# Performance work log

Measured on AMD Instinct MI355X. Metric: run time of the kernel, lower is better.

The kernel has to match this reference:

```python
import jax, jax.numpy as jnp
import numpy as np

B, H, SQ, SKV, D = 2, 16, 2048, 2048, 64
SCALE = 8  # sqrt(head_dim)


def setup_inputs() -> dict:
    key = jax.random.key(0)
    kq, kk, kv, km = jax.random.split(key, 4)
    q = jax.random.normal(kq, (B, H, SQ, D), dtype=jnp.float32)
    k = jax.random.normal(kk, (B, H, SKV, D), dtype=jnp.float32)
    v = jax.random.normal(kv, (B, H, SKV, D), dtype=jnp.float32)
    mask = jax.random.normal(km, (1, 1, SQ, SKV), dtype=jnp.float32)
    return {"q": q, "k": k, "v": v, "mask": mask, "scale": SCALE}


def reference(q, k, v, mask, scale):
    # scores: [B, H, SQ, SKV]
    scores = jnp.einsum("bhqd,bhkd->bhqk", q, k) / scale
    scores = scores + mask  # broadcast additive mask
    probs = jax.nn.softmax(scores, axis=-1)
    # hidden: [B, H, SQ, D]
    return jnp.einsum("bhqk,bhkd->bhqd", probs, v)
```

## Files before the change

### kernel.cpp

```cpp
#include <hip/hip_runtime.h>
#include <hip/hip_bf16.h>

#define NB 2
#define NH 16
#define NSQ 2048
#define NSKV 2048
#define ND 64
#define NT (NSKV / 64)
#define LOG2E 1.4426950408889634f
#define BHSTRIDE (NSKV * ND)

typedef __attribute__((ext_vector_type(8))) short bf16x8;
typedef __attribute__((ext_vector_type(4))) float f32x4;
typedef __attribute__((address_space(1))) const unsigned gas_u32;
typedef __attribute__((address_space(3))) unsigned las_u32;

__device__ __forceinline__ short f2bf(float x) {
  union { float f; unsigned u; } c; c.f = x;
  unsigned r = c.u + 0x7fffu + ((c.u >> 16) & 1u);
  return (short)(r >> 16);
}
__device__ __forceinline__ unsigned pack_bf2(float lo, float hi) {
  union { __hip_bfloat162 h; unsigned u; } c;
  c.h = __float22bfloat162_rn(float2{lo, hi});
  return c.u;
}
__device__ __forceinline__ float u2f(unsigned u) {
  union { unsigned u; float f; } c; c.u = u; return c.f;
}
__device__ __forceinline__ float exp2_fast(float x) {
#if __has_builtin(__builtin_amdgcn_exp2f)
  return __builtin_amdgcn_exp2f(x);
#else
  return exp2f(x);
#endif
}

__device__ __forceinline__ int kvmap(int x) {
  return (x & 3) | (((x >> 4) & 1) << 2) | (((x >> 2) & 1) << 3)
       | (((x >> 3) & 1) << 4) | (x & 32);
}

__global__ void prep_k(const float* __restrict__ K, short* __restrict__ Kp) {
  const int bh = blockIdx.y, tile = blockIdx.x, tid = (int)threadIdx.x;
#pragma unroll
  for (int h = 0; h < 2; ++h) {
    const int u    = tid + h * 256;
    const int nt   = u >> 7, kc = (u >> 6) & 1, lane = u & 63;
    const int prow = nt * 16 + (lane & 15);
    const float* src = K + ((size_t)bh * NSKV + tile * 64 + kvmap(prow)) * ND
                         + kc * 32 + (lane >> 4) * 8;
    float4 a = *(const float4*)src, b = *(const float4*)(src + 4);
    bf16x8 w;
    w[0]=f2bf(a.x); w[1]=f2bf(a.y); w[2]=f2bf(a.z); w[3]=f2bf(a.w);
    w[4]=f2bf(b.x); w[5]=f2bf(b.y); w[6]=f2bf(b.z); w[7]=f2bf(b.w);
    *(bf16x8*)(Kp + (size_t)bh * BHSTRIDE + (size_t)tile * 4096 + u * 8) = w;
  }
}

__global__ void prep_vt(const float* __restrict__ V, short* __restrict__ Vp) {
  __shared__ float T[64][65];
  const int kv0 = blockIdx.x * 64;
  const int bh  = blockIdx.y;
  const int t   = (int)threadIdx.x;
  const float* src = V + ((size_t)bh * NSKV + kv0) * ND;
#pragma unroll
  for (int i = 0; i < 4; ++i) {
    float4 v = *(const float4*)(src + (size_t)((t >> 4) + 16 * i) * ND + (t & 15) * 4);
    T[(t >> 4) + 16 * i][(t & 15) * 4 + 0] = v.x;
    T[(t >> 4) + 16 * i][(t & 15) * 4 + 1] = v.y;
    T[(t >> 4) + 16 * i][(t & 15) * 4 + 2] = v.z;
    T[(t >> 4) + 16 * i][(t & 15) * 4 + 3] = v.w;
  }
  __syncthreads();
  const int d = t >> 2, c = t & 3;
  bf16x8 w0, w1;
#pragma unroll
  for (int j = 0; j < 8; ++j) w0[j] = f2bf(T[c * 16 + j][d]);
#pragma unroll
  for (int j = 0; j < 8; ++j) w1[j] = f2bf(T[c * 16 + 8 + j][d]);
  const int frag  = (d >> 4) * 2 + (c >> 1);
  const int lane0 = (((2 * c) & 3) << 4) | (d & 15);
  const int lane1 = (((2 * c + 1) & 3) << 4) | (d & 15);
  short* dstb = Vp + (size_t)bh * BHSTRIDE + (size_t)blockIdx.x * 4096 + frag * 512;
  *(bf16x8*)(dstb + lane0 * 8) = w0;
  *(bf16x8*)(dstb + lane1 * 8) = w1;
}

__global__ void prep_mt(const float* __restrict__ M, unsigned short* __restrict__ Mt) {
  const int qt = blockIdx.x, kt = blockIdx.y, t = (int)threadIdx.x;
  const int rl = t >> 4, c = t & 15;
  const int row = qt * 16 + rl;
  float4 v = *(const float4*)(M + (size_t)row * NSKV + kt * 64 + c * 4);
  const int nt   = 2 * (c >> 3) + (c & 1);
  const int lq   = (c >> 1) & 3;
  const int lane = lq * 16 + rl;
  ushort4 o;
  o.x = (unsigned short)f2bf(LOG2E * v.x);
  o.y = (unsigned short)f2bf(LOG2E * v.y);
  o.z = (unsigned short)f2bf(LOG2E * v.z);
  o.w = (unsigned short)f2bf(LOG2E * v.w);
  *(ushort4*)(Mt + (((size_t)qt * 32 + kt) * 64 + lane) * 16 + nt * 4) = o;
}

__global__ __launch_bounds__(256, 2)
void attn_fwd(const float* __restrict__ Q, const short* __restrict__ Kp,
              const short* __restrict__ Vp, const unsigned short* __restrict__ Mt,
              const void* __restrict__ scale_p, float* __restrict__ O)
{
  const int lin = (int)blockIdx.x + ((int)blockIdx.y << 4);
  const int swz = ((lin & 7) << 6) | (lin >> 3);
  const int qb  = swz & 15;
  const int bh  = swz >> 4;

  const int tid = (int)threadIdx.x;
  const int wv  = tid >> 6;
  const int ln  = tid & 63;
  const int l16 = ln & 15;
  const int lq  = ln >> 4;

  float scale_v;
  {
    union { int i; float f; } u;
    u.i = ((const int*)scale_p)[0];
    float af = fabsf(u.f);
    scale_v = (af >= 1e-6f && af <= 1e6f) ? u.f : (float)u.i;
  }
  const float qmul = LOG2E / scale_v;

  const int q0 = qb * 128;
  const short* Kb = Kp + (size_t)bh * BHSTRIDE;
  const short* Vb = Vp + (size_t)bh * BHSTRIDE;

  __shared__ short Kl[2][4096];
  __shared__ short Vl[2][4096];

  bf16x8 qf[2][2];
#pragma unroll
  for (int qs = 0; qs < 2; ++qs) {
    const float* qrow = Q + ((size_t)bh * NSQ + q0 + wv * 32 + qs * 16 + l16) * ND;
#pragma unroll
    for (int kc = 0; kc < 2; ++kc) {
      const float4* p = (const float4*)(qrow + kc * 32 + lq * 8);
      float4 a = p[0], b = p[1];
      bf16x8 f;
      f[0]=f2bf(a.x*qmul); f[1]=f2bf(a.y*qmul); f[2]=f2bf(a.z*qmul); f[3]=f2bf(a.w*qmul);
      f[4]=f2bf(b.x*qmul); f[5]=f2bf(b.y*qmul); f[6]=f2bf(b.z*qmul); f[7]=f2bf(b.w*qmul);
      qf[qs][kc] = f;
    }
  }

  f32x4 oa[2][4];
  f32x4 lacc[2];
#pragma unroll
  for (int qs = 0; qs < 2; ++qs) {
#pragma unroll
    for (int dt = 0; dt < 4; ++dt) { f32x4 z = {0.f,0.f,0.f,0.f}; oa[qs][dt] = z; }
    f32x4 z = {0.f,0.f,0.f,0.f}; lacc[qs] = z;
  }

  bf16x8 ones;
#pragma unroll
  for (int j = 0; j < 8; ++j) ones[j] = (short)0x3F80;

  const unsigned short* M0 = Mt + (size_t)(qb * 8 + wv * 2) * 32768 + (size_t)ln * 16;
  const unsigned short* M1 = M0 + 32768;

  auto mload = [&](int t, float4* mf0, float4* mf1) {
    const unsigned short* p0 = M0 + (size_t)t * 1024;
    const unsigned short* p1 = M1 + (size_t)t * 1024;
    uint4 a0 = *(const uint4*)p0, b0 = *(const uint4*)(p0 + 8);
    uint4 a1 = *(const uint4*)p1, b1 = *(const uint4*)(p1 + 8);
    const unsigned u0[8] = {a0.x,a0.y,a0.z,a0.w,b0.x,b0.y,b0.z,b0.w};
    const unsigned u1[8] = {a1.x,a1.y,a1.z,a1.w,b1.x,b1.y,b1.z,b1.w};
#pragma unroll
    for (int nt = 0; nt < 4; ++nt) {
      mf0[nt] = float4{u2f(u0[nt*2] << 16), u2f(u0[nt*2] & 0xffff0000u),
                       u2f(u0[nt*2+1] << 16), u2f(u0[nt*2+1] & 0xffff0000u)};
      mf1[nt] = float4{u2f(u1[nt*2] << 16), u2f(u1[nt*2] & 0xffff0000u),
                       u2f(u1[nt*2+1] << 16), u2f(u1[nt*2+1] & 0xffff0000u)};
    }
  };

  auto stage = [&](int t, int buf) {
    const short* ks = Kb + (size_t)t * 4096;
    const short* vs = Vb + (size_t)t * 4096;
#pragma unroll
    for (int i = 0; i < 2; ++i) {
      const int chunk = wv * 2 + i;
      __builtin_amdgcn_global_load_lds((gas_u32*)(ks + chunk * 512 + ln * 8),
                                       (las_u32*)&Kl[buf][chunk * 512], 16, 0, 0);
      __builtin_amdgcn_global_load_lds((gas_u32*)(vs + chunk * 512 + ln * 8),
                                       (las_u32*)&Vl[buf][chunk * 512], 16, 0, 0);
    }
  };

  auto subtile = [&](bf16x8 (&kf)[4][2], bf16x8 (&vf)[4][2], int qs, float4* mf) {
    f32x4 s[4];
    __builtin_amdgcn_s_setprio(1);
#pragma unroll
    for (int nt = 0; nt < 4; ++nt) {
      f32x4 a = *(const f32x4*)&mf[nt];
      a = __builtin_amdgcn_mfma_f32_16x16x32_bf16(kf[nt][0], qf[qs][0], a, 0, 0, 0);
      a = __builtin_amdgcn_mfma_f32_16x16x32_bf16(kf[nt][1], qf[qs][1], a, 0, 0, 0);
      s[nt] = a;
    }
    __builtin_amdgcn_s_setprio(0);
#pragma unroll
    for (int nt = 0; nt < 4; ++nt) {
      s[nt][0] = exp2_fast(s[nt][0]);
      s[nt][1] = exp2_fast(s[nt][1]);
      s[nt][2] = exp2_fast(s[nt][2]);
      s[nt][3] = exp2_fast(s[nt][3]);
    }
    bf16x8 pa[2];
#pragma unroll
    for (int kc = 0; kc < 2; ++kc) {
      union { unsigned u[4]; bf16x8 v; } w;
      w.u[0] = pack_bf2(s[2*kc][0],   s[2*kc][1]);
      w.u[1] = pack_bf2(s[2*kc][2],   s[2*kc][3]);
      w.u[2] = pack_bf2(s[2*kc+1][0], s[2*kc+1][1]);
      w.u[3] = pack_bf2(s[2*kc+1][2], s[2*kc+1][3]);
      pa[kc] = w.v;
    }
    __builtin_amdgcn_s_setprio(1);
#pragma unroll
    for (int kc = 0; kc < 2; ++kc) {
#pragma unroll
      for (int dt = 0; dt < 4; ++dt)
        oa[qs][dt] = __builtin_amdgcn_mfma_f32_16x16x32_bf16(pa[kc], vf[dt][kc], oa[qs][dt], 0, 0, 0);
      lacc[qs] = __builtin_amdgcn_mfma_f32_16x16x32_bf16(pa[kc], ones, lacc[qs], 0, 0, 0);
    }
    __builtin_amdgcn_s_setprio(0);
  };

  auto tile = [&](int t, int buf, float4 (&mc0)[4], float4 (&mc1)[4],
                  float4 (&mn0)[4], float4 (&mn1)[4]) {
    if (t + 1 < NT) {
      stage(t + 1, buf ^ 1);
      mload(t + 1, mn0, mn1);
    }
    bf16x8 kf[4][2], vf[4][2];
#pragma unroll
    for (int nt = 0; nt < 4; ++nt)
#pragma unroll
      for (int kc = 0; kc < 2; ++kc) {
        kf[nt][kc] = *(const bf16x8*)&Kl[buf][(nt * 2 + kc) * 512 + ln * 8];
        vf[nt][kc] = *(const bf16x8*)&Vl[buf][(nt * 2 + kc) * 512 + ln * 8];
      }
    subtile(kf, vf, 0, mc0);
    subtile(kf, vf, 1, mc1);
    __syncthreads();
  };

  float4 mA0[4], mA1[4], mB0[4], mB1[4];
  stage(0, 0);
  mload(0, mA0, mA1);
  __syncthreads();

  for (int t = 0; t < NT; t += 2) {
    tile(t,     0, mA0, mA1, mB0, mB1);
    tile(t + 1, 1, mB0, mB1, mA0, mA1);
  }

#pragma unroll
  for (int qs = 0; qs < 2; ++qs)
#pragma unroll
    for (int r = 0; r < 4; ++r) {
      const float inv = 1.0f / lacc[qs][r];
      float* orow = O + ((size_t)bh * NSQ + q0 + wv * 32 + qs * 16 + lq * 4 + r) * ND;
#pragma unroll
      for (int dt = 0; dt < 4; ++dt)
        orow[dt * 16 + l16] = oa[qs][dt][r] * inv;
    }
}

extern "C" void kernel_launch(void* const* d_in, const int* in_sizes, int n_in,
                              void* d_out, int out_size, void* d_ws, size_t ws_size,
                              hipStream_t stream) {
  const float* q     = (const float*)d_in[0];
  const float* k     = (const float*)d_in[1];
  const float* v     = (const float*)d_in[2];
  const float* mask  = (const float*)d_in[3];
  const void*  scale = (const void*)d_in[4];
  float* out = (float*)d_out;

  const size_t NELEM = (size_t)NB * NH * NSKV * ND;
  short* Kpk = (short*)d_ws;
  short* Vpk = Kpk + NELEM;
  unsigned short* Mtl = (unsigned short*)(Vpk + NELEM);

  prep_k<<<dim3(NSKV / 64, NB * NH), 256, 0, stream>>>(k, Kpk);
  prep_vt<<<dim3(NSKV / 64, NB * NH), 256, 0, stream>>>(v, Vpk);
  prep_mt<<<dim3(NSQ / 16, NSKV / 64), 256, 0, stream>>>(mask, Mtl);

  dim3 grid(NSQ / 128, NB * NH);
  attn_fwd<<<grid, 256, 0, stream>>>(q, Kpk, Vpk, Mtl, scale, out);
}
```

Before: 72.34 us.

## Use 512-thread blocks with one 16-row query slice per wave

```diff
diff --git a/kernel.cpp b/kernel.cpp
--- a/kernel.cpp
+++ b/kernel.cpp
@@ -103,15 +103,15 @@
   *(ushort4*)(Mt + (((size_t)qt * 32 + kt) * 64 + lane) * 16 + nt * 4) = o;
 }
 
-__global__ __launch_bounds__(256, 2)
+__global__ __launch_bounds__(512, 4)
 void attn_fwd(const float* __restrict__ Q, const short* __restrict__ Kp,
               const short* __restrict__ Vp, const unsigned short* __restrict__ Mt,
               const void* __restrict__ scale_p, float* __restrict__ O)
 {
-  const int lin = (int)blockIdx.x + ((int)blockIdx.y << 4);
-  const int swz = ((lin & 7) << 6) | (lin >> 3);
-  const int qb  = swz & 15;
-  const int bh  = swz >> 4;
+  const int lin = (int)blockIdx.x;
+  const int j   = lin & 7, m = lin >> 3;
+  const int qb  = 2 * j + (m & 1);
+  const int bh  = m >> 1;
 
   const int tid = (int)threadIdx.x;
   const int wv  = tid >> 6;
@@ -135,10 +135,9 @@
   __shared__ short Kl[2][4096];
   __shared__ short Vl[2][4096];
 
-  bf16x8 qf[2][2];
-#pragma unroll
-  for (int qs = 0; qs < 2; ++qs) {
-    const float* qrow = Q + ((size_t)bh * NSQ + q0 + wv * 32 + qs * 16 + l16) * ND;
+  bf16x8 qf[2];
+  {
+    const float* qrow = Q + ((size_t)bh * NSQ + q0 + wv * 16 + l16) * ND;
 #pragma unroll
     for (int kc = 0; kc < 2; ++kc) {
       const float4* p = (const float4*)(qrow + kc * 32 + lq * 8);
@@ -146,63 +145,62 @@
       bf16x8 f;
       f[0]=f2bf(a.x*qmul); f[1]=f2bf(a.y*qmul); f[2]=f2bf(a.z*qmul); f[3]=f2bf(a.w*qmul);
       f[4]=f2bf(b.x*qmul); f[5]=f2bf(b.y*qmul); f[6]=f2bf(b.z*qmul); f[7]=f2bf(b.w*qmul);
-      qf[qs][kc] = f;
-    }
-  }
-
-  f32x4 oa[2][4];
-  f32x4 lacc[2];
-#pragma unroll
-  for (int qs = 0; qs < 2; ++qs) {
-#pragma unroll
-    for (int dt = 0; dt < 4; ++dt) { f32x4 z = {0.f,0.f,0.f,0.f}; oa[qs][dt] = z; }
-    f32x4 z = {0.f,0.f,0.f,0.f}; lacc[qs] = z;
-  }
+      qf[kc] = f;
+    }
+  }
+
+  f32x4 oa[4];
+  f32x4 lacc;
+#pragma unroll
+  for (int dt = 0; dt < 4; ++dt) { f32x4 z = {0.f,0.f,0.f,0.f}; oa[dt] = z; }
+  { f32x4 z = {0.f,0.f,0.f,0.f}; lacc = z; }
 
   bf16x8 ones;
 #pragma unroll
-  for (int j = 0; j < 8; ++j) ones[j] = (short)0x3F80;
-
-  const unsigned short* M0 = Mt + (size_t)(qb * 8 + wv * 2) * 32768 + (size_t)ln * 16;
-  const unsigned short* M1 = M0 + 32768;
-
-  auto mload = [&](int t, float4* mf0, float4* mf1) {
+  for (int j2 = 0; j2 < 8; ++j2) ones[j2] = (short)0x3F80;
+
+  const unsigned short* M0 = Mt + (size_t)(qb * 8 + wv) * 32768 + (size_t)ln * 16;
+
+  union MU { uint4 q[2]; unsigned u[8]; };
+
+  auto mload = [&](int t, MU& mu) {
     const unsigned short* p0 = M0 + (size_t)t * 1024;
-    const unsigned short* p1 = M1 + (size_t)t * 1024;
-    uint4 a0 = *(const uint4*)p0, b0 = *(const uint4*)(p0 + 8);
-    uint4 a1 = *(const uint4*)p1, b1 = *(const uint4*)(p1 + 8);
-    const unsigned u0[8] = {a0.x,a0.y,a0.z,a0.w,b0.x,b0.y,b0.z,b0.w};
-    const unsigned u1[8] = {a1.x,a1.y,a1.z,a1.w,b1.x,b1.y,b1.z,b1.w};
-#pragma unroll
-    for (int nt = 0; nt < 4; ++nt) {
-      mf0[nt] = float4{u2f(u0[nt*2] << 16), u2f(u0[nt*2] & 0xffff0000u),
-                       u2f(u0[nt*2+1] << 16), u2f(u0[nt*2+1] & 0xffff0000u)};
-      mf1[nt] = float4{u2f(u1[nt*2] << 16), u2f(u1[nt*2] & 0xffff0000u),
-                       u2f(u1[nt*2+1] << 16), u2f(u1[nt*2+1] & 0xffff0000u)};
-    }
+    mu.q[0] = *(const uint4*)p0;
+    mu.q[1] = *(const uint4*)(p0 + 8);
   };
 
   auto stage = [&](int t, int buf) {
     const short* ks = Kb + (size_t)t * 4096;
     const short* vs = Vb + (size_t)t * 4096;
-#pragma unroll
-    for (int i = 0; i < 2; ++i) {
-      const int chunk = wv * 2 + i;
-      __builtin_amdgcn_global_load_lds((gas_u32*)(ks + chunk * 512 + ln * 8),
-                                       (las_u32*)&Kl[buf][chunk * 512], 16, 0, 0);
-      __builtin_amdgcn_global_load_lds((gas_u32*)(vs + chunk * 512 + ln * 8),
-                                       (las_u32*)&Vl[buf][chunk * 512], 16, 0, 0);
-    }
+    __builtin_amdgcn_global_load_lds((gas_u32*)(ks + wv * 512 + ln * 8),
+                                     (las_u32*)&Kl[buf][wv * 512], 16, 0, 0);
+    __builtin_amdgcn_global_load_lds((gas_u32*)(vs + wv * 512 + ln * 8),
+                                     (las_u32*)&Vl[buf][wv * 512], 16, 0, 0);
   };
 
-  auto subtile = [&](bf16x8 (&kf)[4][2], bf16x8 (&vf)[4][2], int qs, float4* mf) {
+  auto tile = [&](int t, int buf, MU& mc, MU& mn) {
+    if (t + 1 < NT) {
+      stage(t + 1, buf ^ 1);
+      mload(t + 1, mn);
+    }
+    bf16x8 kf[4][2], vf[4][2];
+#pragma unroll
+    for (int nt = 0; nt < 4; ++nt)
+#pragma unroll
+      for (int kc = 0; kc < 2; ++kc) {
+        kf[nt][kc] = *(const bf16x8*)&Kl[buf][(nt * 2 + kc) * 512 + ln * 8];
+        vf[nt][kc] = *(const bf16x8*)&Vl[buf][(nt * 2 + kc) * 512 + ln * 8];
+      }
     f32x4 s[4];
     __builtin_amdgcn_s_setprio(1);
 #pragma unroll
     for (int nt = 0; nt < 4; ++nt) {
-      f32x4 a = *(const f32x4*)&mf[nt];
-      a = __builtin_amdgcn_mfma_f32_16x16x32_bf16(kf[nt][0], qf[qs][0], a, 0, 0, 0);
-      a = __builtin_amdgcn_mfma_f32_16x16x32_bf16(kf[nt][1], qf[qs][1], a, 0, 0, 0);
+      const unsigned w0 = mc.u[nt * 2], w1 = mc.u[nt * 2 + 1];
+      f32x4 a;
+      a[0] = u2f(w0 << 16); a[1] = u2f(w0 & 0xffff0000u);
+      a[2] = u2f(w1 << 16); a[3] = u2f(w1 & 0xffff0000u);
+      a = __builtin_amdgcn_mfma_f32_16x16x32_bf16(kf[nt][0], qf[0], a, 0, 0, 0);
+      a = __builtin_amdgcn_mfma_f32_16x16x32_bf16(kf[nt][1], qf[1], a, 0, 0, 0);
       s[nt] = a;
     }
     __builtin_amdgcn_s_setprio(0);
@@ -228,51 +226,31 @@
     for (int kc = 0; kc < 2; ++kc) {
 #pragma unroll
       for (int dt = 0; dt < 4; ++dt)
-        oa[qs][dt] = __builtin_amdgcn_mfma_f32_16x16x32_bf16(pa[kc], vf[dt][kc], oa[qs][dt], 0, 0, 0);
-      lacc[qs] = __builtin_amdgcn_mfma_f32_16x16x32_bf16(pa[kc], ones, lacc[qs], 0, 0, 0);
+        oa[dt] = __builtin_amdgcn_mfma_f32_16x16x32_bf16(pa[kc], vf[dt][kc], oa[dt], 0, 0, 0);
+      lacc = __builtin_amdgcn_mfma_f32_16x16x32_bf16(pa[kc], ones, lacc, 0, 0, 0);
     }
     __builtin_amdgcn_s_setprio(0);
-  };
-
-  auto tile = [&](int t, int buf, float4 (&mc0)[4], float4 (&mc1)[4],
-                  float4 (&mn0)[4], float4 (&mn1)[4]) {
-    if (t + 1 < NT) {
-      stage(t + 1, buf ^ 1);
-      mload(t + 1, mn0, mn1);
-    }
-    bf16x8 kf[4][2], vf[4][2];
-#pragma unroll
-    for (int nt = 0; nt < 4; ++nt)
-#pragma unroll
-      for (int kc = 0; kc < 2; ++kc) {
-        kf[nt][kc] = *(const bf16x8*)&Kl[buf][(nt * 2 + kc) * 512 + ln * 8];
-        vf[nt][kc] = *(const bf16x8*)&Vl[buf][(nt * 2 + kc) * 512 + ln * 8];
-      }
-    subtile(kf, vf, 0, mc0);
-    subtile(kf, vf, 1, mc1);
     __syncthreads();
   };
 
-  float4 mA0[4], mA1[4], mB0[4], mB1[4];
+  MU mA, mB;
   stage(0, 0);
-  mload(0, mA0, mA1);
+  mload(0, mA);
   __syncthreads();
 
   for (int t = 0; t < NT; t += 2) {
-    tile(t,     0, mA0, mA1, mB0, mB1);
-    tile(t + 1, 1, mB0, mB1, mA0, mA1);
-  }
-
-#pragma unroll
-  for (int qs = 0; qs < 2; ++qs)
-#pragma unroll
-    for (int r = 0; r < 4; ++r) {
-      const float inv = 1.0f / lacc[qs][r];
-      float* orow = O + ((size_t)bh * NSQ + q0 + wv * 32 + qs * 16 + lq * 4 + r) * ND;
-#pragma unroll
-      for (int dt = 0; dt < 4; ++dt)
-        orow[dt * 16 + l16] = oa[qs][dt][r] * inv;
-    }
+    tile(t,     0, mA, mB);
+    tile(t + 1, 1, mB, mA);
+  }
+
+#pragma unroll
+  for (int r = 0; r < 4; ++r) {
+    const float inv = 1.0f / lacc[r];
+    float* orow = O + ((size_t)bh * NSQ + q0 + wv * 16 + lq * 4 + r) * ND;
+#pragma unroll
+    for (int dt = 0; dt < 4; ++dt)
+      orow[dt * 16 + l16] = oa[dt][r] * inv;
+  }
 }
 
 extern "C" void kernel_launch(void* const* d_in, const int* in_sizes, int n_in,
@@ -294,6 +272,5 @@
   prep_vt<<<dim3(NSKV / 64, NB * NH), 256, 0, stream>>>(v, Vpk);
   prep_mt<<<dim3(NSQ / 16, NSKV / 64), 256, 0, stream>>>(mask, Mtl);
 
-  dim3 grid(NSQ / 128, NB * NH);
-  attn_fwd<<<grid, 256, 0, stream>>>(q, Kpk, Vpk, Mtl, scale, out);
-}
+  attn_fwd<<<dim3(512), 512, 0, stream>>>(q, Kpk, Vpk, Mtl, scale, out);
+}
```

New measurement: 77.87 us. 7.6% more time.

## Pack two heads per 512-thread block and defer mask unpacking to use

Applied to the files above, without the earlier changes.

```diff
diff --git a/kernel.cpp b/kernel.cpp
--- a/kernel.cpp
+++ b/kernel.cpp
@@ -103,21 +103,24 @@
   *(ushort4*)(Mt + (((size_t)qt * 32 + kt) * 64 + lane) * 16 + nt * 4) = o;
 }
 
-__global__ __launch_bounds__(256, 2)
+__global__ __launch_bounds__(512, 2)
 void attn_fwd(const float* __restrict__ Q, const short* __restrict__ Kp,
               const short* __restrict__ Vp, const unsigned short* __restrict__ Mt,
               const void* __restrict__ scale_p, float* __restrict__ O)
 {
-  const int lin = (int)blockIdx.x + ((int)blockIdx.y << 4);
-  const int swz = ((lin & 7) << 6) | (lin >> 3);
+  const int lin = (int)blockIdx.x;
+  const int swz = ((lin & 7) << 5) | (lin >> 3);
   const int qb  = swz & 15;
-  const int bh  = swz >> 4;
+  const int bhp = swz >> 4;
 
   const int tid = (int)threadIdx.x;
   const int wv  = tid >> 6;
+  const int wg  = wv >> 2;
+  const int wl  = wv & 3;
   const int ln  = tid & 63;
   const int l16 = ln & 15;
   const int lq  = ln >> 4;
+  const int bh  = bhp * 2 + wg;
 
   float scale_v;
   {
@@ -129,16 +132,18 @@
   const float qmul = LOG2E / scale_v;
 
   const int q0 = qb * 128;
-  const short* Kb = Kp + (size_t)bh * BHSTRIDE;
-  const short* Vb = Vp + (size_t)bh * BHSTRIDE;
-
-  __shared__ short Kl[2][4096];
-  __shared__ short Vl[2][4096];
+  const short* Kb0 = Kp + (size_t)(bhp * 2)     * BHSTRIDE;
+  const short* Kb1 = Kp + (size_t)(bhp * 2 + 1) * BHSTRIDE;
+  const short* Vb0 = Vp + (size_t)(bhp * 2)     * BHSTRIDE;
+  const short* Vb1 = Vp + (size_t)(bhp * 2 + 1) * BHSTRIDE;
+
+  __shared__ short Ksh[2][2][4096];
+  __shared__ short Vsh[2][2][4096];
 
   bf16x8 qf[2][2];
 #pragma unroll
   for (int qs = 0; qs < 2; ++qs) {
-    const float* qrow = Q + ((size_t)bh * NSQ + q0 + wv * 32 + qs * 16 + l16) * ND;
+    const float* qrow = Q + ((size_t)bh * NSQ + q0 + wl * 32 + qs * 16 + l16) * ND;
 #pragma unroll
     for (int kc = 0; kc < 2; ++kc) {
       const float4* p = (const float4*)(qrow + kc * 32 + lq * 8);
@@ -163,44 +168,45 @@
 #pragma unroll
   for (int j = 0; j < 8; ++j) ones[j] = (short)0x3F80;
 
-  const unsigned short* M0 = Mt + (size_t)(qb * 8 + wv * 2) * 32768 + (size_t)ln * 16;
+  const unsigned short* M0 = Mt + (size_t)(qb * 8 + wl * 2) * 32768 + (size_t)ln * 16;
   const unsigned short* M1 = M0 + 32768;
 
-  auto mload = [&](int t, float4* mf0, float4* mf1) {
+  union MU { uint4 q[2]; unsigned u[8]; };
+
+  auto mload = [&](int t, MU& m0, MU& m1) {
     const unsigned short* p0 = M0 + (size_t)t * 1024;
     const unsigned short* p1 = M1 + (size_t)t * 1024;
-    uint4 a0 = *(const uint4*)p0, b0 = *(const uint4*)(p0 + 8);
-    uint4 a1 = *(const uint4*)p1, b1 = *(const uint4*)(p1 + 8);
-    const unsigned u0[8] = {a0.x,a0.y,a0.z,a0.w,b0.x,b0.y,b0.z,b0.w};
-    const unsigned u1[8] = {a1.x,a1.y,a1.z,a1.w,b1.x,b1.y,b1.z,b1.w};
-#pragma unroll
-    for (int nt = 0; nt < 4; ++nt) {
-      mf0[nt] = float4{u2f(u0[nt*2] << 16), u2f(u0[nt*2] & 0xffff0000u),
-                       u2f(u0[nt*2+1] << 16), u2f(u0[nt*2+1] & 0xffff0000u)};
-      mf1[nt] = float4{u2f(u1[nt*2] << 16), u2f(u1[nt*2] & 0xffff0000u),
-                       u2f(u1[nt*2+1] << 16), u2f(u1[nt*2+1] & 0xffff0000u)};
-    }
+    m0.q[0] = *(const uint4*)p0;
+    m0.q[1] = *(const uint4*)(p0 + 8);
+    m1.q[0] = *(const uint4*)p1;
+    m1.q[1] = *(const uint4*)(p1 + 8);
   };
 
   auto stage = [&](int t, int buf) {
-    const short* ks = Kb + (size_t)t * 4096;
-    const short* vs = Vb + (size_t)t * 4096;
-#pragma unroll
-    for (int i = 0; i < 2; ++i) {
-      const int chunk = wv * 2 + i;
-      __builtin_amdgcn_global_load_lds((gas_u32*)(ks + chunk * 512 + ln * 8),
-                                       (las_u32*)&Kl[buf][chunk * 512], 16, 0, 0);
-      __builtin_amdgcn_global_load_lds((gas_u32*)(vs + chunk * 512 + ln * 8),
-                                       (las_u32*)&Vl[buf][chunk * 512], 16, 0, 0);
+#pragma unroll
+    for (int j = 0; j < 4; ++j) {
+      const int c    = wv * 4 + j;
+      const int g2   = c >> 4;
+      const int rem  = c & 15;
+      const int isV  = rem >> 3;
+      const int off8 = (rem & 7) * 512;
+      const short* kb = g2 ? Kb1 : Kb0;
+      const short* vb = g2 ? Vb1 : Vb0;
+      const short* src = (isV ? vb : kb) + (size_t)t * 4096 + off8 + ln * 8;
+      short* dst = isV ? &Vsh[g2][buf][off8] : &Ksh[g2][buf][off8];
+      __builtin_amdgcn_global_load_lds((gas_u32*)src, (las_u32*)dst, 16, 0, 0);
     }
   };
 
-  auto subtile = [&](bf16x8 (&kf)[4][2], bf16x8 (&vf)[4][2], int qs, float4* mf) {
+  auto subtile = [&](bf16x8 (&kf)[4][2], bf16x8 (&vf)[4][2], int qs, MU& mc) {
     f32x4 s[4];
     __builtin_amdgcn_s_setprio(1);
 #pragma unroll
     for (int nt = 0; nt < 4; ++nt) {
-      f32x4 a = *(const f32x4*)&mf[nt];
+      const unsigned w0 = mc.u[nt * 2], w1 = mc.u[nt * 2 + 1];
+      f32x4 a;
+      a[0] = u2f(w0 << 16); a[1] = u2f(w0 & 0xffff0000u);
+      a[2] = u2f(w1 << 16); a[3] = u2f(w1 & 0xffff0000u);
       a = __builtin_amdgcn_mfma_f32_16x16x32_bf16(kf[nt][0], qf[qs][0], a, 0, 0, 0);
       a = __builtin_amdgcn_mfma_f32_16x16x32_bf16(kf[nt][1], qf[qs][1], a, 0, 0, 0);
       s[nt] = a;
@@ -234,8 +240,7 @@
     __builtin_amdgcn_s_setprio(0);
   };
 
-  auto tile = [&](int t, int buf, float4 (&mc0)[4], float4 (&mc1)[4],
-                  float4 (&mn0)[4], float4 (&mn1)[4]) {
+  auto tile = [&](int t, int buf, MU& mc0, MU& mc1, MU& mn0, MU& mn1) {
     if (t + 1 < NT) {
       stage(t + 1, buf ^ 1);
       mload(t + 1, mn0, mn1);
@@ -245,15 +250,15 @@
     for (int nt = 0; nt < 4; ++nt)
 #pragma unroll
       for (int kc = 0; kc < 2; ++kc) {
-        kf[nt][kc] = *(const bf16x8*)&Kl[buf][(nt * 2 + kc) * 512 + ln * 8];
-        vf[nt][kc] = *(const bf16x8*)&Vl[buf][(nt * 2 + kc) * 512 + ln * 8];
+        kf[nt][kc] = *(const bf16x8*)&Ksh[wg][buf][(nt * 2 + kc) * 512 + ln * 8];
+        vf[nt][kc] = *(const bf16x8*)&Vsh[wg][buf][(nt * 2 + kc) * 512 + ln * 8];
       }
     subtile(kf, vf, 0, mc0);
     subtile(kf, vf, 1, mc1);
     __syncthreads();
   };
 
-  float4 mA0[4], mA1[4], mB0[4], mB1[4];
+  MU mA0, mA1, mB0, mB1;
   stage(0, 0);
   mload(0, mA0, mA1);
   __syncthreads();
@@ -268,7 +273,7 @@
 #pragma unroll
     for (int r = 0; r < 4; ++r) {
       const float inv = 1.0f / lacc[qs][r];
-      float* orow = O + ((size_t)bh * NSQ + q0 + wv * 32 + qs * 16 + lq * 4 + r) * ND;
+      float* orow = O + ((size_t)bh * NSQ + q0 + wl * 32 + qs * 16 + lq * 4 + r) * ND;
 #pragma unroll
       for (int dt = 0; dt < 4; ++dt)
         orow[dt * 16 + l16] = oa[qs][dt][r] * inv;
@@ -294,6 +299,5 @@
   prep_vt<<<dim3(NSKV / 64, NB * NH), 256, 0, stream>>>(v, Vpk);
   prep_mt<<<dim3(NSQ / 16, NSKV / 64), 256, 0, stream>>>(mask, Mtl);
 
-  dim3 grid(NSQ / 128, NB * NH);
-  attn_fwd<<<grid, 256, 0, stream>>>(q, Kpk, Vpk, Mtl, scale, out);
-}
+  attn_fwd<<<dim3(256), 512, 0, stream>>>(q, Kpk, Vpk, Mtl, scale, out);
+}
```

Measured after the change: 76.92 us. 1.06x slower.
